# Performance work log

Hardware: AMD Instinct MI355X
Metric: run time of the kernel (lower is better)

## Reference

```python
import jax, jax.numpy as jnp
import numpy as np

D_MODEL = 1024
D_FF = 4096
NUM_EXPERTS = 8
TOP_K = 2
SEQ = 1024
BATCH = 2


def setup_inputs() -> dict:
    key = jax.random.key(0)
    ks = jax.random.split(key, 7)
    s = 0.02
    x = jax.random.normal(ks[0], (SEQ, BATCH, D_MODEL), dtype=jnp.float32)
    gate_w = jax.random.normal(ks[1], (D_MODEL, NUM_EXPERTS), dtype=jnp.float32) * s
    gate_b = jnp.zeros((NUM_EXPERTS,), dtype=jnp.float32)
    W1 = jax.random.normal(ks[2], (NUM_EXPERTS, D_MODEL, D_FF), dtype=jnp.float32) * s
    b1 = jnp.zeros((NUM_EXPERTS, D_FF), dtype=jnp.float32)
    W2 = jax.random.normal(ks[3], (NUM_EXPERTS, D_FF, D_MODEL), dtype=jnp.float32) * s
    b2 = jnp.zeros((NUM_EXPERTS, D_MODEL), dtype=jnp.float32)
    return {"x": x, "gate_w": gate_w, "gate_b": gate_b,
            "W1": W1, "b1": b1, "W2": W2, "b2": b2}


def reference(x, gate_w, gate_b, W1, b1, W2, b2):
    S, B, D = x.shape
    x_flat = x.reshape(-1, D)                       # [T, D], T = S*B
    scores = x_flat @ gate_w + gate_b               # [T, E]
    topk_vals, topk_idx = jax.lax.top_k(scores, TOP_K)   # [T, K]
    topk_probs = jax.nn.softmax(topk_vals, axis=-1)      # [T, K]
    # combine weight per (token, expert): sum of probs over slots routed to e
    one_hot = jax.nn.one_hot(topk_idx, NUM_EXPERTS, dtype=x.dtype)  # [T, K, E]
    combine = jnp.einsum('tk,tke->te', topk_probs, one_hot)         # [T, E]
    # dense per-expert FFN (tokens with combine weight 0 contribute nothing,
    # matching the masked gather/scatter in the torch loop)
    h = jax.nn.relu(jnp.einsum('td,edf->etf', x_flat, W1) + b1[:, None, :])  # [E, T, F]
    y = jnp.einsum('etf,efd->etd', h, W2) + b2[:, None, :]                    # [E, T, D]
    out = jnp.einsum('te,etd->td', combine, y)       # [T, D]
    return out.reshape(S, B, D)
```

## Files before the change

kernel.cpp:

```cpp
#include <hip/hip_runtime.h>
#include <stdint.h>

#define T_TOKENS 2048
#define DM 1024
#define DF 4096
#define NEXP 8
#define NSLOTS (T_TOKENS * 2)

typedef __bf16 bf16x8 __attribute__((ext_vector_type(8)));
typedef float f32x4 __attribute__((ext_vector_type(4)));

__device__ __forceinline__ ushort f2bf(float f) {
    union { float f; uint32_t u; } v; v.f = f;
    uint32_t r = v.u + 0x7FFFu + ((v.u >> 16) & 1u);
    return (ushort)(r >> 16);
}

__device__ __forceinline__ void gload16(const ushort* g, ushort* l) {
    __builtin_amdgcn_global_load_lds(
        (const __attribute__((address_space(1))) uint32_t*)g,
        (__attribute__((address_space(3))) uint32_t*)l,
        16, 0, 0);
}

__global__ void init_cnt(uint32_t* cnt) {
    if (threadIdx.x < NEXP) cnt[threadIdx.x] = 0;
}

__global__ void prefix_offs(const uint32_t* __restrict__ cnt,
                            uint32_t* __restrict__ offs)
{
    if (threadIdx.x == 0) {
        uint32_t a = 0;
#pragma unroll
        for (int e = 0; e < NEXP; ++e) { offs[e] = a; a += cnt[e]; }
        offs[NEXP] = a;
    }
}

__global__ __launch_bounds__(256) void prep_kernel(
    const float* __restrict__ x, const float* __restrict__ gw,
    const float* __restrict__ gb,
    uint32_t* __restrict__ route, uint32_t* __restrict__ cnt,
    float* __restrict__ prob, uint32_t* __restrict__ epk,
    ushort* __restrict__ xb)
{
    const int bx = blockIdx.x;
    const int tid = threadIdx.x;

    if (bx < 512) {
        const int w = tid >> 6;
        const int lane = tid & 63;
        const int t = bx * 4 + w;
        float acc[NEXP];
#pragma unroll
        for (int e = 0; e < NEXP; ++e) acc[e] = 0.f;
        const float* xr = x + (size_t)t * DM;
#pragma unroll
        for (int j = 0; j < DM / 64; ++j) {
            const int d = j * 64 + lane;
            const float xv = xr[d];
            const float* g = gw + (size_t)d * NEXP;
#pragma unroll
            for (int e = 0; e < NEXP; ++e) acc[e] += xv * g[e];
        }
#pragma unroll
        for (int e = 0; e < NEXP; ++e) {
#pragma unroll
            for (int off = 32; off > 0; off >>= 1)
                acc[e] += __shfl_xor(acc[e], off);
            acc[e] += gb[e];
        }
        if (lane == 0) {
            int e0 = 0; float v0 = acc[0];
#pragma unroll
            for (int e = 1; e < NEXP; ++e) if (acc[e] > v0) { v0 = acc[e]; e0 = e; }
            int e1 = -1; float v1 = -1e30f;
#pragma unroll
            for (int e = 0; e < NEXP; ++e) if (e != e0 && acc[e] > v1) { v1 = acc[e]; e1 = e; }
            const float ex = expf(v1 - v0);
            const float inv = 1.f / (1.f + ex);
            prob[t * 2 + 0] = inv;
            prob[t * 2 + 1] = ex * inv;
            uint32_t pos = atomicAdd(&cnt[e0], 1u);
            route[e0 * T_TOKENS + pos] = (uint32_t)(t * 2);
            epk[t * 2] = ((uint32_t)e0 << 16) | pos;
            pos = atomicAdd(&cnt[e1], 1u);
            route[e1 * T_TOKENS + pos] = (uint32_t)(t * 2 + 1);
            epk[t * 2 + 1] = ((uint32_t)e1 << 16) | pos;
        }
    } else {
        const int i = ((bx - 512) * 256 + tid) * 4;
        const float4 v = *reinterpret_cast<const float4*>(x + i);
        ushort4 o;
        o.x = f2bf(v.x); o.y = f2bf(v.y); o.z = f2bf(v.z); o.w = f2bf(v.w);
        *reinterpret_cast<ushort4*>(xb + i) = o;
    }
}

template<int KD, int ND, bool FIRST, int SPLIT, int NMT, int NT>
__global__ __launch_bounds__(256, 4) void moe_gemm12(
    const ushort* __restrict__ Abuf,
    const float* __restrict__ W,
    const float* __restrict__ bias,
    const uint32_t* __restrict__ route,
    const uint32_t* __restrict__ cnt,
    const uint32_t* __restrict__ offs,
    const float* __restrict__ prob,
    ushort* __restrict__ hout,
    float* __restrict__ yout)
{
    const int bx0 = blockIdx.x;
    const int cpx = (NEXP * NMT * NT) >> 3;
    const int wk  = (bx0 & 7) * cpx + (bx0 >> 3);
    const int e   = wk / (NMT * NT);
    const int r   = wk % (NMT * NT);
    const int nt  = r / NMT;
    const int mt  = r % NMT;
    const uint32_t cntE = cnt[e];
    const int m0 = mt * 128;
    if ((uint32_t)m0 >= cntE) return;
    const uint32_t hb = offs[e];
    const int n0 = nt * 128;
    const int z  = (SPLIT > 1) ? (int)blockIdx.z : 0;
    const int kbeg = z * (KD / SPLIT);
    const int niter = (KD / SPLIT) / 32;

    __shared__ ushort As[2][128 * 32];
    __shared__ ushort Bs[2][128 * 40];
    __shared__ uint32_t s_route[128];
    __shared__ float s_p[128];

    const int tid = threadIdx.x;
    if (FIRST) {
        if (tid < 128) {
            const uint32_t idx = (uint32_t)(m0 + tid);
            const uint32_t s = (idx < cntE) ? route[e * T_TOKENS + idx] : 0u;
            s_route[tid] = s;
            s_p[tid] = prob[s];
        }
        __syncthreads();
    }

    const int w = tid >> 6, l = tid & 63;

    const ushort* asrc[2];
#pragma unroll
    for (int i = 0; i < 2; ++i) {
        const int chunk = (w * 2 + i) * 64 + l;
        const int row = chunk >> 2;
        const int c   = chunk & 3;
        const int cs  = c ^ ((row >> 1) & 3);
        size_t arow;
        if (FIRST) arow = (size_t)(s_route[row] >> 1);
        else       arow = (size_t)(hb + m0 + row);
        asrc[i] = Abuf + arow * KD + cs * 8 + kbeg;
    }

    const int c4 = tid & 31;
    const int kq = tid >> 5;
    const float* wbase = W + ((size_t)e * KD + kbeg + (size_t)kq * 4) * ND
                         + n0 + c4 * 4;
    ushort* const bdst0 = &Bs[0][0];

    f32x4 acc[4][4];
#pragma unroll
    for (int i = 0; i < 4; ++i)
#pragma unroll
        for (int j = 0; j < 4; ++j) acc[i][j] = (f32x4){0.f, 0.f, 0.f, 0.f};

    const int q = l & 15, g = l >> 4;
    const int wm = w >> 1, wn = w & 1;

    int aoff[4], boff[4];
#pragma unroll
    for (int mi = 0; mi < 4; ++mi) {
        int row = wm * 64 + mi * 16 + q;
        aoff[mi] = row * 64 + (g ^ ((row >> 1) & 3)) * 16;
        row = wn * 64 + mi * 16 + q;
        boff[mi] = row * 40 + g * 8;
    }

    ushort* const abase0 = &As[0][0];

    {
        float4 b0 = *reinterpret_cast<const float4*>(wbase + (size_t)0 * ND);
        float4 b1 = *reinterpret_cast<const float4*>(wbase + (size_t)1 * ND);
        float4 b2 = *reinterpret_cast<const float4*>(wbase + (size_t)2 * ND);
        float4 b3 = *reinterpret_cast<const float4*>(wbase + (size_t)3 * ND);
#pragma unroll
        for (int i = 0; i < 2; ++i) gload16(asrc[i], abase0 + (w * 2 + i) * 512);
        const int bn = c4 * 4;
        ushort4 o0 = { f2bf(b0.x), f2bf(b1.x), f2bf(b2.x), f2bf(b3.x) };
        ushort4 o1 = { f2bf(b0.y), f2bf(b1.y), f2bf(b2.y), f2bf(b3.y) };
        ushort4 o2 = { f2bf(b0.z), f2bf(b1.z), f2bf(b2.z), f2bf(b3.z) };
        ushort4 o3 = { f2bf(b0.w), f2bf(b1.w), f2bf(b2.w), f2bf(b3.w) };
        *reinterpret_cast<ushort4*>(bdst0 + (bn + 0) * 40 + kq * 4) = o0;
        *reinterpret_cast<ushort4*>(bdst0 + (bn + 1) * 40 + kq * 4) = o1;
        *reinterpret_cast<ushort4*>(bdst0 + (bn + 2) * 40 + kq * 4) = o2;
        *reinterpret_cast<ushort4*>(bdst0 + (bn + 3) * 40 + kq * 4) = o3;
    }
    __syncthreads();

    int cur = 0;
    for (int t = 0; t < niter; ++t) {
        float4 b0, b1, b2, b3;
        const bool pf = (t + 1 < niter);
        if (pf) {
            const size_t k1 = (size_t)(t + 1) * 32;
            b0 = *reinterpret_cast<const float4*>(wbase + (k1 + 0) * ND);
            b1 = *reinterpret_cast<const float4*>(wbase + (k1 + 1) * ND);
            b2 = *reinterpret_cast<const float4*>(wbase + (k1 + 2) * ND);
            b3 = *reinterpret_cast<const float4*>(wbase + (k1 + 3) * ND);
            ushort* ad = abase0 + (cur ^ 1) * (128 * 32) + (w * 2) * 512;
#pragma unroll
            for (int i = 0; i < 2; ++i) gload16(asrc[i] + k1, ad + i * 512);
        }

        const char* Ab = (const char*)(abase0 + cur * (128 * 32));
        const ushort* Bb = bdst0 + cur * (128 * 40);
        bf16x8 af[4], bv[4];
#pragma unroll
        for (int mi = 0; mi < 4; ++mi)
            af[mi] = *reinterpret_cast<const bf16x8*>(Ab + aoff[mi]);
#pragma unroll
        for (int ni = 0; ni < 4; ++ni)
            bv[ni] = *reinterpret_cast<const bf16x8*>(Bb + boff[ni]);
        __builtin_amdgcn_s_setprio(1);
#pragma unroll
        for (int mi = 0; mi < 4; ++mi)
#pragma unroll
            for (int ni = 0; ni < 4; ++ni)
                acc[mi][ni] = __builtin_amdgcn_mfma_f32_16x16x32_bf16(
                    af[mi], bv[ni], acc[mi][ni], 0, 0, 0);
        __builtin_amdgcn_s_setprio(0);
        __builtin_amdgcn_sched_barrier(0);

        if (pf) {
            ushort* bd = bdst0 + (cur ^ 1) * (128 * 40);
            const int bn = c4 * 4;
            ushort4 o0 = { f2bf(b0.x), f2bf(b1.x), f2bf(b2.x), f2bf(b3.x) };
            ushort4 o1 = { f2bf(b0.y), f2bf(b1.y), f2bf(b2.y), f2bf(b3.y) };
            ushort4 o2 = { f2bf(b0.z), f2bf(b1.z), f2bf(b2.z), f2bf(b3.z) };
            ushort4 o3 = { f2bf(b0.w), f2bf(b1.w), f2bf(b2.w), f2bf(b3.w) };
            *reinterpret_cast<ushort4*>(bd + (bn + 0) * 40 + kq * 4) = o0;
            *reinterpret_cast<ushort4*>(bd + (bn + 1) * 40 + kq * 4) = o1;
            *reinterpret_cast<ushort4*>(bd + (bn + 2) * 40 + kq * 4) = o2;
            *reinterpret_cast<ushort4*>(bd + (bn + 3) * 40 + kq * 4) = o3;
        }
        __syncthreads();
        cur ^= 1;
    }

#pragma unroll
    for (int mi = 0; mi < 4; ++mi) {
#pragma unroll
        for (int ni = 0; ni < 4; ++ni) {
            const int gcol = n0 + wn * 64 + ni * 16 + q;
#pragma unroll
            for (int j = 0; j < 4; ++j) {
                const int row = wm * 64 + mi * 16 + g * 4 + j;
                if ((uint32_t)(m0 + row) < cntE) {
                    const size_t grow = (size_t)(hb + m0 + row);
                    if (FIRST) {
                        float v = acc[mi][ni][j] + bias[e * ND + gcol];
                        v = fmaxf(v, 0.f) * s_p[row];
                        hout[grow * ND + gcol] = f2bf(v);
                    } else {
                        yout[((size_t)z * NSLOTS + grow) * ND + gcol] = acc[mi][ni][j];
                    }
                }
            }
        }
    }
}

__global__ __launch_bounds__(256) void combine5(
    const float* __restrict__ yc, const uint32_t* __restrict__ epk,
    const uint32_t* __restrict__ offs, const float* __restrict__ prob,
    const float* __restrict__ b2, float* __restrict__ out)
{
    const int gid = blockIdx.x * 256 + threadIdx.x;
    const int t = gid >> 8;
    const int dq = gid & 255;
    const uint32_t p0 = epk[2 * t], p1 = epk[2 * t + 1];
    const uint32_t e0 = p0 >> 16, e1 = p1 >> 16;
    const uint32_t r0 = offs[e0] + (p0 & 0xFFFFu);
    const uint32_t r1 = offs[e1] + (p1 & 0xFFFFu);
    const float w0 = prob[2 * t], w1 = prob[2 * t + 1];
    const float4 bb0 = reinterpret_cast<const float4*>(b2 + (size_t)e0 * DM)[dq];
    const float4 bb1 = reinterpret_cast<const float4*>(b2 + (size_t)e1 * DM)[dq];
    float4 o = { w0 * bb0.x + w1 * bb1.x, w0 * bb0.y + w1 * bb1.y,
                 w0 * bb0.z + w1 * bb1.z, w0 * bb0.w + w1 * bb1.w };
    const float4* Y = reinterpret_cast<const float4*>(yc);
#pragma unroll
    for (int zz = 0; zz < 4; ++zz) {
        const float4 a = Y[((size_t)zz * NSLOTS + r0) * 256 + dq];
        const float4 b = Y[((size_t)zz * NSLOTS + r1) * 256 + dq];
        o.x += a.x + b.x; o.y += a.y + b.y; o.z += a.z + b.z; o.w += a.w + b.w;
    }
    reinterpret_cast<float4*>(out)[gid] = o;
}

__global__ __launch_bounds__(256) void gate_route_fb(
    const float* __restrict__ x, const float* __restrict__ gw,
    const float* __restrict__ gb,
    uint32_t* __restrict__ route, uint32_t* __restrict__ cnt,
    float* __restrict__ prob)
{
    const int w = threadIdx.x >> 6;
    const int lane = threadIdx.x & 63;
    const int t = blockIdx.x * 4 + w;
    float acc[NEXP];
#pragma unroll
    for (int e = 0; e < NEXP; ++e) acc[e] = 0.f;
    const float* xr = x + (size_t)t * DM;
#pragma unroll
    for (int j = 0; j < DM / 64; ++j) {
        const int d = j * 64 + lane;
        const float xv = xr[d];
        const float* g = gw + (size_t)d * NEXP;
#pragma unroll
        for (int e = 0; e < NEXP; ++e) acc[e] += xv * g[e];
    }
#pragma unroll
    for (int e = 0; e < NEXP; ++e) {
#pragma unroll
        for (int off = 32; off > 0; off >>= 1)
            acc[e] += __shfl_xor(acc[e], off);
        acc[e] += gb[e];
    }
    if (lane == 0) {
        int e0 = 0; float v0 = acc[0];
#pragma unroll
        for (int e = 1; e < NEXP; ++e) if (acc[e] > v0) { v0 = acc[e]; e0 = e; }
        int e1 = -1; float v1 = -1e30f;
#pragma unroll
        for (int e = 0; e < NEXP; ++e) if (e != e0 && acc[e] > v1) { v1 = acc[e]; e1 = e; }
        const float ex = expf(v1 - v0);
        const float inv = 1.f / (1.f + ex);
        prob[t * 2 + 0] = inv;
        prob[t * 2 + 1] = ex * inv;
        uint32_t pos = atomicAdd(&cnt[e0], 1u);
        route[e0 * T_TOKENS + pos] = (uint32_t)(t * 2);
        pos = atomicAdd(&cnt[e1], 1u);
        route[e1 * T_TOKENS + pos] = (uint32_t)(t * 2 + 1);
    }
}

__global__ __launch_bounds__(256) void convert_x_fb(const float* __restrict__ x,
                                                    ushort* __restrict__ xb)
{
    const int i = (blockIdx.x * 256 + threadIdx.x) * 4;
    const float4 v = *reinterpret_cast<const float4*>(x + i);
    ushort4 o;
    o.x = f2bf(v.x); o.y = f2bf(v.y); o.z = f2bf(v.z); o.w = f2bf(v.w);
    *reinterpret_cast<ushort4*>(xb + i) = o;
}

template<int KD, int ND, bool FIRST>
__global__ __launch_bounds__(256) void moe_gemm_v1(
    const ushort* __restrict__ Abuf, const float* __restrict__ W,
    const float* __restrict__ bias, const uint32_t* __restrict__ route,
    const uint32_t* __restrict__ cnt, const float* __restrict__ prob,
    ushort* __restrict__ hout, float* __restrict__ yout)
{
    const int e = blockIdx.x >> 4;
    const int mt = blockIdx.x & 15;
    const uint32_t cntE = cnt[e];
    const int m0 = mt * 128;
    if ((uint32_t)m0 >= cntE) return;
    const int n0 = blockIdx.y * 128;
    const int tid = threadIdx.x;
    __shared__ ushort Asm[128][40];
    __shared__ ushort Bsm[128][40];
    __shared__ uint32_t s_route[128];
    if (tid < 128) {
        const uint32_t idx = (uint32_t)(m0 + tid);
        s_route[tid] = (idx < cntE) ? route[e * T_TOKENS + idx] : 0xFFFFFFFFu;
    }
    __syncthreads();
    const int ar = tid >> 1, ah = tid & 1;
    const uint32_t s_a = s_route[ar];
    size_t arow = 0;
    if (s_a != 0xFFFFFFFFu) arow = FIRST ? (size_t)(s_a >> 1) : (size_t)s_a;
    const ushort* asrc = Abuf + arow * KD + ah * 16;
    const int c4 = tid & 31, kq = tid >> 5;
    const float* wbase = W + (size_t)e * KD * ND + (size_t)n0 + (size_t)c4 * 4;
    f32x4 acc[4][4];
#pragma unroll
    for (int i = 0; i < 4; ++i)
#pragma unroll
        for (int j = 0; j < 4; ++j) acc[i][j] = (f32x4){0.f, 0.f, 0.f, 0.f};
    const int lane = tid & 63, wv = tid >> 6;
    const int wm = wv >> 1, wn = wv & 1;
    const int q = lane & 15, g = lane >> 4;
    for (int k0 = 0; k0 < KD; k0 += 32) {
        {
            const uint4* src = reinterpret_cast<const uint4*>(asrc + k0);
            const uint4 v0 = src[0];
            const uint4 v1 = src[1];
            *reinterpret_cast<uint4*>(&Asm[ar][ah * 16]) = v0;
            *reinterpret_cast<uint4*>(&Asm[ar][ah * 16 + 8]) = v1;
        }
        {
            ushort vals[4][4];
#pragma unroll
            for (int r = 0; r < 4; ++r) {
                const float4 v = *reinterpret_cast<const float4*>(
                    wbase + (size_t)(k0 + kq * 4 + r) * ND);
                vals[r][0] = f2bf(v.x); vals[r][1] = f2bf(v.y);
                vals[r][2] = f2bf(v.z); vals[r][3] = f2bf(v.w);
            }
#pragma unroll
            for (int c = 0; c < 4; ++c) {
                const ushort4 o = { vals[0][c], vals[1][c], vals[2][c], vals[3][c] };
                *reinterpret_cast<ushort4*>(&Bsm[c4 * 4 + c][kq * 4]) = o;
            }
        }
        __syncthreads();
        bf16x8 af[4], bfr[4];
#pragma unroll
        for (int mi = 0; mi < 4; ++mi)
            af[mi] = *reinterpret_cast<const bf16x8*>(&Asm[wm * 64 + mi * 16 + q][g * 8]);
#pragma unroll
        for (int ni = 0; ni < 4; ++ni)
            bfr[ni] = *reinterpret_cast<const bf16x8*>(&Bsm[wn * 64 + ni * 16 + q][g * 8]);
#pragma unroll
        for (int mi = 0; mi < 4; ++mi)
#pragma unroll
            for (int ni = 0; ni < 4; ++ni)
                acc[mi][ni] = __builtin_amdgcn_mfma_f32_16x16x32_bf16(
                    af[mi], bfr[ni], acc[mi][ni], 0, 0, 0);
        __syncthreads();
    }
#pragma unroll
    for (int mi = 0; mi < 4; ++mi) {
#pragma unroll
        for (int ni = 0; ni < 4; ++ni) {
            const int gcol = n0 + wn * 64 + ni * 16 + q;
#pragma unroll
            for (int j = 0; j < 4; ++j) {
                const int row = wm * 64 + mi * 16 + g * 4 + j;
                if ((uint32_t)(m0 + row) < cntE) {
                    const uint32_t s = s_route[row];
                    float v = acc[mi][ni][j] + bias[e * ND + gcol];
                    if (FIRST) {
                        v = fmaxf(v, 0.f);
                        hout[(size_t)s * ND + gcol] = f2bf(v);
                    } else {
                        yout[(size_t)s * ND + gcol] = v * prob[s];
                    }
                }
            }
        }
    }
}

__global__ __launch_bounds__(256) void combine1(const float* __restrict__ yc,
                                                float* __restrict__ out)
{
    const int gid = blockIdx.x * 256 + threadIdx.x;
    const int t = gid >> 8;
    const int dq = gid & 255;
    const float4 va = reinterpret_cast<const float4*>(yc)[(size_t)(2 * t) * 256 + dq];
    const float4 vb = reinterpret_cast<const float4*>(yc)[(size_t)(2 * t + 1) * 256 + dq];
    const float4 o = { va.x + vb.x, va.y + vb.y, va.z + vb.z, va.w + vb.w };
    reinterpret_cast<float4*>(out)[gid] = o;
}

extern "C" void kernel_launch(void* const* d_in, const int* in_sizes, int n_in,
                              void* d_out, int out_size, void* d_ws, size_t ws_size,
                              hipStream_t stream)
{
    const float* x  = (const float*)d_in[0];
    const float* gw = (const float*)d_in[1];
    const float* gb = (const float*)d_in[2];
    const float* W1 = (const float*)d_in[3];
    const float* b1 = (const float*)d_in[4];
    const float* W2 = (const float*)d_in[5];
    const float* b2 = (const float*)d_in[6];
    float* out = (float*)d_out;
    char* ws = (char*)d_ws;

    const size_t OFF_XB    = 0;
    const size_t OFF_H     = 4194304;
    const size_t OFF_ROUTE = 38797312;
    const size_t OFF_CNT   = 38862848;
    const size_t OFF_OFFS  = 38862912;
    const size_t OFF_PROB  = 38862976;
    const size_t OFF_EPK   = 38879360;
    const size_t OFF_YC    = 41943040;
    const size_t NEED      = 109051904ull;

    if (ws_size >= NEED) {
        ushort*   xb    = (ushort*)(ws + OFF_XB);
        ushort*   h     = (ushort*)(ws + OFF_H);
        float*    yc    = (float*)(ws + OFF_YC);
        uint32_t* route = (uint32_t*)(ws + OFF_ROUTE);
        uint32_t* cnt   = (uint32_t*)(ws + OFF_CNT);
        uint32_t* offs  = (uint32_t*)(ws + OFF_OFFS);
        float*    prob  = (float*)(ws + OFF_PROB);
        uint32_t* epk   = (uint32_t*)(ws + OFF_EPK);

        hipLaunchKernelGGL(init_cnt, dim3(1), dim3(64), 0, stream, cnt);
        hipLaunchKernelGGL(prep_kernel, dim3(2560), dim3(256), 0, stream,
                           x, gw, gb, route, cnt, prob, epk, xb);
        hipLaunchKernelGGL(prefix_offs, dim3(1), dim3(64), 0, stream, cnt, offs);
        hipLaunchKernelGGL((moe_gemm12<DM, DF, true, 1, 16, 32>),
                           dim3(NEXP * 16 * 32, 1, 1), dim3(256), 0, stream,
                           xb, W1, b1, route, cnt, offs, prob, h, (float*)nullptr);
        hipLaunchKernelGGL((moe_gemm12<DF, DM, false, 4, 16, 8>),
                           dim3(NEXP * 16 * 8, 1, 4), dim3(256), 0, stream,
                           h, W2, (const float*)nullptr, route, cnt, offs,
                           (const float*)nullptr, (ushort*)nullptr, yc);
        hipLaunchKernelGGL(combine5, dim3(T_TOKENS * DM / 1024), dim3(256), 0, stream,
                           yc, epk, offs, prob, b2, out);
    } else {
        const size_t F_XB = 0, F_H = 4194304, F_YC = 37748736;
        const size_t F_ROUTE = 54525952, F_CNT = 54591488, F_PROB = 54591552;
        ushort*   xb    = (ushort*)(ws + F_XB);
        ushort*   h     = (ushort*)(ws + F_H);
        float*    yc    = (float*)(ws + F_YC);
        uint32_t* route = (uint32_t*)(ws + F_ROUTE);
        uint32_t* cnt   = (uint32_t*)(ws + F_CNT);
        float*    prob  = (float*)(ws + F_PROB);

        hipLaunchKernelGGL(init_cnt, dim3(1), dim3(64), 0, stream, cnt);
        hipLaunchKernelGGL(gate_route_fb, dim3(T_TOKENS / 4), dim3(256), 0, stream,
                           x, gw, gb, route, cnt, prob);
        hipLaunchKernelGGL(convert_x_fb, dim3(T_TOKENS * DM / 1024), dim3(256), 0, stream, x, xb);
        hipLaunchKernelGGL((moe_gemm_v1<DM, DF, true>), dim3(NEXP * 16, DF / 128),
                           dim3(256), 0, stream, xb, W1, b1, route, cnt, prob,
                           h, (float*)nullptr);
        hipLaunchKernelGGL((moe_gemm_v1<DF, DM, false>), dim3(NEXP * 16, DM / 128),
                           dim3(256), 0, stream, h, W2, b2, route, cnt, prob,
                           (ushort*)nullptr, yc);
        hipLaunchKernelGGL(combine1, dim3(T_TOKENS * DM / 1024), dim3(256), 0, stream, yc, out);
    }
}
```

Measured before the change: 338.2 us.

## Stream fp32 weights to LDS via direct async loads and convert at fragment read

```diff
diff --git a/kernel.cpp b/kernel.cpp
--- a/kernel.cpp
+++ b/kernel.cpp
@@ -17,6 +17,13 @@
 }
 
 __device__ __forceinline__ void gload16(const ushort* g, ushort* l) {
+    __builtin_amdgcn_global_load_lds(
+        (const __attribute__((address_space(1))) uint32_t*)g,
+        (__attribute__((address_space(3))) uint32_t*)l,
+        16, 0, 0);
+}
+
+__device__ __forceinline__ void gload16f(const float* g, float* l) {
     __builtin_amdgcn_global_load_lds(
         (const __attribute__((address_space(1))) uint32_t*)g,
         (__attribute__((address_space(3))) uint32_t*)l,
@@ -99,7 +106,7 @@
 }
 
 template<int KD, int ND, bool FIRST, int SPLIT, int NMT, int NT>
-__global__ __launch_bounds__(256, 4) void moe_gemm12(
+__global__ __launch_bounds__(256, 3) void moe_gemm14(
     const ushort* __restrict__ Abuf,
     const float* __restrict__ W,
     const float* __restrict__ bias,
@@ -127,7 +134,7 @@
     const int niter = (KD / SPLIT) / 32;
 
     __shared__ ushort As[2][128 * 32];
-    __shared__ ushort Bs[2][128 * 40];
+    __shared__ float  Bs[2][32 * 128];
     __shared__ uint32_t s_route[128];
     __shared__ float s_p[128];
 
@@ -157,11 +164,16 @@
         asrc[i] = Abuf + arow * KD + cs * 8 + kbeg;
     }
 
-    const int c4 = tid & 31;
-    const int kq = tid >> 5;
-    const float* wbase = W + ((size_t)e * KD + kbeg + (size_t)kq * 4) * ND
-                         + n0 + c4 * 4;
-    ushort* const bdst0 = &Bs[0][0];
+    const float* bsrc[4];
+#pragma unroll
+    for (int i = 0; i < 4; ++i) {
+        const int chunk = (w * 4 + i) * 64 + l;
+        const int kk = chunk >> 5;
+        const int cc = chunk & 31;
+        const int cs = cc ^ (((kk >> 3) & 1) << 2);
+        bsrc[i] = W + ((size_t)e * KD + kbeg + kk) * ND + n0 + cs * 4;
+    }
+    const size_t BADV = (size_t)32 * ND;
 
     f32x4 acc[4][4];
 #pragma unroll
@@ -172,60 +184,60 @@
     const int q = l & 15, g = l >> 4;
     const int wm = w >> 1, wn = w & 1;
 
-    int aoff[4], boff[4];
+    int aoff[4];
 #pragma unroll
     for (int mi = 0; mi < 4; ++mi) {
-        int row = wm * 64 + mi * 16 + q;
+        const int row = wm * 64 + mi * 16 + q;
         aoff[mi] = row * 64 + (g ^ ((row >> 1) & 3)) * 16;
-        row = wn * 64 + mi * 16 + q;
-        boff[mi] = row * 40 + g * 8;
+    }
+    int boffB[4];
+#pragma unroll
+    for (int ni = 0; ni < 4; ++ni) {
+        const int n = wn * 64 + ni * 16 + q;
+        boffB[ni] = g * 8 * 128 + (((n >> 2) ^ ((g & 1) << 2)) << 2) + (n & 3);
     }
 
     ushort* const abase0 = &As[0][0];
-
-    {
-        float4 b0 = *reinterpret_cast<const float4*>(wbase + (size_t)0 * ND);
-        float4 b1 = *reinterpret_cast<const float4*>(wbase + (size_t)1 * ND);
-        float4 b2 = *reinterpret_cast<const float4*>(wbase + (size_t)2 * ND);
-        float4 b3 = *reinterpret_cast<const float4*>(wbase + (size_t)3 * ND);
-#pragma unroll
-        for (int i = 0; i < 2; ++i) gload16(asrc[i], abase0 + (w * 2 + i) * 512);
-        const int bn = c4 * 4;
-        ushort4 o0 = { f2bf(b0.x), f2bf(b1.x), f2bf(b2.x), f2bf(b3.x) };
-        ushort4 o1 = { f2bf(b0.y), f2bf(b1.y), f2bf(b2.y), f2bf(b3.y) };
-        ushort4 o2 = { f2bf(b0.z), f2bf(b1.z), f2bf(b2.z), f2bf(b3.z) };
-        ushort4 o3 = { f2bf(b0.w), f2bf(b1.w), f2bf(b2.w), f2bf(b3.w) };
-        *reinterpret_cast<ushort4*>(bdst0 + (bn + 0) * 40 + kq * 4) = o0;
-        *reinterpret_cast<ushort4*>(bdst0 + (bn + 1) * 40 + kq * 4) = o1;
-        *reinterpret_cast<ushort4*>(bdst0 + (bn + 2) * 40 + kq * 4) = o2;
-        *reinterpret_cast<ushort4*>(bdst0 + (bn + 3) * 40 + kq * 4) = o3;
-    }
-    __syncthreads();
+    float*  const bbase0 = &Bs[0][0];
+
+#pragma unroll
+    for (int i = 0; i < 2; ++i) gload16(asrc[i], abase0 + (w * 2 + i) * 512);
+#pragma unroll
+    for (int i = 0; i < 4; ++i) gload16f(bsrc[i], bbase0 + (w * 4 + i) * 256);
 
     int cur = 0;
+#pragma unroll 1
     for (int t = 0; t < niter; ++t) {
-        float4 b0, b1, b2, b3;
-        const bool pf = (t + 1 < niter);
-        if (pf) {
-            const size_t k1 = (size_t)(t + 1) * 32;
-            b0 = *reinterpret_cast<const float4*>(wbase + (k1 + 0) * ND);
-            b1 = *reinterpret_cast<const float4*>(wbase + (k1 + 1) * ND);
-            b2 = *reinterpret_cast<const float4*>(wbase + (k1 + 2) * ND);
-            b3 = *reinterpret_cast<const float4*>(wbase + (k1 + 3) * ND);
+        if (t + 1 < niter) {
             ushort* ad = abase0 + (cur ^ 1) * (128 * 32) + (w * 2) * 512;
+            float*  bd = bbase0 + (cur ^ 1) * (32 * 128) + (w * 4) * 256;
+            const int k1 = (t + 1) * 32;
 #pragma unroll
             for (int i = 0; i < 2; ++i) gload16(asrc[i] + k1, ad + i * 512);
-        }
-
-        const char* Ab = (const char*)(abase0 + cur * (128 * 32));
-        const ushort* Bb = bdst0 + cur * (128 * 40);
+#pragma unroll
+            for (int i = 0; i < 4; ++i) gload16f(bsrc[i] + (size_t)(t + 1) * BADV,
+                                                 bd + i * 256);
+            asm volatile("s_waitcnt vmcnt(6)" ::: "memory");
+        } else {
+            asm volatile("s_waitcnt vmcnt(0)" ::: "memory");
+        }
+        __builtin_amdgcn_s_barrier();
+        __builtin_amdgcn_sched_barrier(0);
+
+        const char*  Ab = (const char*)(abase0 + cur * (128 * 32));
+        const float* Bf = bbase0 + cur * (32 * 128);
         bf16x8 af[4], bv[4];
 #pragma unroll
         for (int mi = 0; mi < 4; ++mi)
             af[mi] = *reinterpret_cast<const bf16x8*>(Ab + aoff[mi]);
 #pragma unroll
-        for (int ni = 0; ni < 4; ++ni)
-            bv[ni] = *reinterpret_cast<const bf16x8*>(Bb + boff[ni]);
+        for (int ni = 0; ni < 4; ++ni) {
+            union { ushort u[8]; bf16x8 v; } bc;
+            const int bb = boffB[ni];
+#pragma unroll
+            for (int j = 0; j < 8; ++j) bc.u[j] = f2bf(Bf[bb + j * 128]);
+            bv[ni] = bc.v;
+        }
         __builtin_amdgcn_s_setprio(1);
 #pragma unroll
         for (int mi = 0; mi < 4; ++mi)
@@ -234,21 +246,7 @@
                 acc[mi][ni] = __builtin_amdgcn_mfma_f32_16x16x32_bf16(
                     af[mi], bv[ni], acc[mi][ni], 0, 0, 0);
         __builtin_amdgcn_s_setprio(0);
-        __builtin_amdgcn_sched_barrier(0);
-
-        if (pf) {
-            ushort* bd = bdst0 + (cur ^ 1) * (128 * 40);
-            const int bn = c4 * 4;
-            ushort4 o0 = { f2bf(b0.x), f2bf(b1.x), f2bf(b2.x), f2bf(b3.x) };
-            ushort4 o1 = { f2bf(b0.y), f2bf(b1.y), f2bf(b2.y), f2bf(b3.y) };
-            ushort4 o2 = { f2bf(b0.z), f2bf(b1.z), f2bf(b2.z), f2bf(b3.z) };
-            ushort4 o3 = { f2bf(b0.w), f2bf(b1.w), f2bf(b2.w), f2bf(b3.w) };
-            *reinterpret_cast<ushort4*>(bd + (bn + 0) * 40 + kq * 4) = o0;
-            *reinterpret_cast<ushort4*>(bd + (bn + 1) * 40 + kq * 4) = o1;
-            *reinterpret_cast<ushort4*>(bd + (bn + 2) * 40 + kq * 4) = o2;
-            *reinterpret_cast<ushort4*>(bd + (bn + 3) * 40 + kq * 4) = o3;
-        }
-        __syncthreads();
+        __builtin_amdgcn_s_barrier();
         cur ^= 1;
     }
 
@@ -275,6 +273,7 @@
     }
 }
 
+template<int SPLIT>
 __global__ __launch_bounds__(256) void combine5(
     const float* __restrict__ yc, const uint32_t* __restrict__ epk,
     const uint32_t* __restrict__ offs, const float* __restrict__ prob,
@@ -294,7 +293,7 @@
                  w0 * bb0.z + w1 * bb1.z, w0 * bb0.w + w1 * bb1.w };
     const float4* Y = reinterpret_cast<const float4*>(yc);
 #pragma unroll
-    for (int zz = 0; zz < 4; ++zz) {
+    for (int zz = 0; zz < SPLIT; ++zz) {
         const float4 a = Y[((size_t)zz * NSLOTS + r0) * 256 + dq];
         const float4 b = Y[((size_t)zz * NSLOTS + r1) * 256 + dq];
         o.x += a.x + b.x; o.y += a.y + b.y; o.z += a.z + b.z; o.w += a.w + b.w;
@@ -491,7 +490,7 @@
     const size_t OFF_PROB  = 38862976;
     const size_t OFF_EPK   = 38879360;
     const size_t OFF_YC    = 41943040;
-    const size_t NEED      = 109051904ull;
+    const size_t NEED      = 75497472ull;
 
     if (ws_size >= NEED) {
         ushort*   xb    = (ushort*)(ws + OFF_XB);
@@ -507,14 +506,14 @@
         hipLaunchKernelGGL(prep_kernel, dim3(2560), dim3(256), 0, stream,
                            x, gw, gb, route, cnt, prob, epk, xb);
         hipLaunchKernelGGL(prefix_offs, dim3(1), dim3(64), 0, stream, cnt, offs);
-        hipLaunchKernelGGL((moe_gemm12<DM, DF, true, 1, 16, 32>),
+        hipLaunchKernelGGL((moe_gemm14<DM, DF, true, 1, 16, 32>),
                            dim3(NEXP * 16 * 32, 1, 1), dim3(256), 0, stream,
                            xb, W1, b1, route, cnt, offs, prob, h, (float*)nullptr);
-        hipLaunchKernelGGL((moe_gemm12<DF, DM, false, 4, 16, 8>),
-                           dim3(NEXP * 16 * 8, 1, 4), dim3(256), 0, stream,
+        hipLaunchKernelGGL((moe_gemm14<DF, DM, false, 2, 16, 8>),
+                           dim3(NEXP * 16 * 8, 1, 2), dim3(256), 0, stream,
                            h, W2, (const float*)nullptr, route, cnt, offs,
                            (const float*)nullptr, (ushort*)nullptr, yc);
-        hipLaunchKernelGGL(combine5, dim3(T_TOKENS * DM / 1024), dim3(256), 0, stream,
+        hipLaunchKernelGGL((combine5<2>), dim3(T_TOKENS * DM / 1024), dim3(256), 0, stream,
                            yc, epk, offs, prob, b2, out);
     } else {
         const size_t F_XB = 0, F_H = 4194304, F_YC = 37748736;
```

Result: slower. 384.5 us (+13.7%).
